# Kernel optimization log

Measured on AMD Instinct MI355X. Metric: run time of the kernel, lower is better.

## Reference

```python
import jax, jax.numpy as jnp
import numpy as np


def _conv(x, w, b=None, stride=1, pad=0):
    y = jax.lax.conv_general_dilated(x, w, (stride, stride), [(pad, pad), (pad, pad)],
                                     dimension_numbers=('NCHW', 'OIHW', 'NCHW'))
    if b is not None:
        y = y + b[None, :, None, None]
    return y


def _slice3d(grid, guide):
    # Trilinear grid_sample, align_corners=False, zero padding.
    # grid: (N, C=12, D=8, GH, GW); guide: (N,1,H,W) in [-1,1]
    N, C, D, GH, GW = grid.shape
    H, W = guide.shape[2], guide.shape[3]
    xs = 2.0 * jnp.arange(W, dtype=grid.dtype) / max(W - 1, 1) - 1.0
    ys = 2.0 * jnp.arange(H, dtype=grid.dtype) / max(H - 1, 1) - 1.0
    gx = ((xs + 1.0) * GW - 1.0) * 0.5               # (W,)
    gy = ((ys + 1.0) * GH - 1.0) * 0.5               # (H,)
    gz = ((guide[:, 0] + 1.0) * D - 1.0) * 0.5       # (N,H,W)
    x0f = jnp.floor(gx); y0f = jnp.floor(gy); z0f = jnp.floor(gz)
    fx = gx - x0f; fy = gy - y0f; fz = gz - z0f
    x0 = x0f.astype(jnp.int32); y0 = y0f.astype(jnp.int32); z0 = z0f.astype(jnp.int32)
    gf = grid.reshape(N, C, D * GH * GW)

    def corner(zi, yi, xi, wz, wy, wx):
        mask = ((zi >= 0) & (zi < D)) & ((yi >= 0) & (yi < GH))[None, :, None] & ((xi >= 0) & (xi < GW))[None, None, :]
        zc = jnp.clip(zi, 0, D - 1); yc = jnp.clip(yi, 0, GH - 1); xc = jnp.clip(xi, 0, GW - 1)
        flat = zc * (GH * GW) + yc[None, :, None] * GW + xc[None, None, :]   # (N,H,W)
        v = jnp.take_along_axis(gf, flat.reshape(N, 1, H * W), axis=2).reshape(N, C, H, W)
        w = (wz * wy[None, :, None] * wx[None, None, :]) * mask.astype(grid.dtype)  # (N,H,W)
        return v * w[:, None]

    out = jnp.zeros((N, C, H, W), grid.dtype)
    for dz in (0, 1):
        for dy in (0, 1):
            for dx in (0, 1):
                out = out + corner(z0 + dz, y0 + dy, x0 + dx,
                                   fz if dz else 1.0 - fz,
                                   fy if dy else 1.0 - fy,
                                   fx if dx else 1.0 - fx)
    return out


def setup_inputs() -> dict:
    key = jax.random.key(0)
    ks = jax.random.split(key, 40)
    def w(i, shape):
        return jax.random.normal(ks[i], shape, jnp.float32) * 0.05
    return {
        'low_res': jax.random.uniform(ks[0], (4, 3, 256, 256), jnp.float32),
        'full_res': jax.random.uniform(ks[1], (4, 1, 1024, 1024), jnp.float32),
        'w0': w(2, (8, 3, 3, 3)), 'b0': w(3, (8,)),
        'w1': w(4, (16, 8, 3, 3)), 'b1': w(5, (16,)),
        'w2': w(6, (32, 16, 3, 3)), 'b2': w(7, (32,)),
        'w3': w(8, (64, 32, 3, 3)), 'b3': w(9, (64,)),
        'wl0': w(10, (64, 64, 3, 3)), 'bl0': w(11, (64,)),
        'wl1': w(12, (64, 64, 3, 3)),
        'wg1': w(13, (128, 64, 3, 3)), 'bg1': w(14, (128,)),
        'wg2': w(15, (256, 128, 3, 3)), 'bg2': w(16, (256,)),
        'wf1': w(17, (256, 448, 1, 1)), 'bf1': w(18, (256,)),
        'wf2': w(19, (128, 256, 1, 1)), 'bf2': w(20, (128,)),
        'wf3': w(21, (64, 128, 1, 1)), 'bf3': w(22, (64,)),
        'wlin': w(23, (96, 64, 1, 1)), 'blin': w(24, (96,)),
        'wgd1': w(25, (16, 1, 3, 3)), 'bgd1': w(26, (16,)),
        'wgd2': w(27, (1, 16, 1, 1)), 'bgd2': w(28, (1,)),
        'wau1': w(29, (16, 1, 1, 1)), 'bau1': w(30, (16,)),
        'wau2': w(31, (1, 16, 1, 1)), 'bau2': w(32, (1,)),
        'wav1': w(33, (16, 1, 1, 1)), 'bav1': w(34, (16,)),
        'wav2': w(35, (1, 16, 1, 1)), 'bav2': w(36, (1,)),
    }


def reference(low_res, full_res, w0, b0, w1, b1, w2, b2, w3, b3, wl0, bl0, wl1,
              wg1, bg1, wg2, bg2, wf1, bf1, wf2, bf2, wf3, bf3, wlin, blin,
              wgd1, bgd1, wgd2, bgd2, wau1, bau1, wau2, bau2, wav1, bav1, wav2, bav2):
    relu = jax.nn.relu
    N = low_res.shape[0]
    H, W = full_res.shape[2], full_res.shape[3]
    fake = jax.image.resize(low_res, (N, 3, H, W), 'bilinear')
    # splat stack: 4 stride-2 convs
    x = relu(_conv(low_res, w0, b0, 2, 1))
    x = relu(_conv(x, w1, b1, 2, 1))
    x = relu(_conv(x, w2, b2, 2, 1))
    splat = relu(_conv(x, w3, b3, 2, 1))                 # (N,64,16,16)
    local = _conv(relu(_conv(splat, wl0, bl0, 1, 1)), wl1, None, 1, 1)
    # global branch
    a0 = splat.mean(axis=(2, 3), keepdims=True)
    x1 = relu(_conv(splat, wg1, bg1, 2, 1))
    a1 = x1.mean(axis=(2, 3), keepdims=True)
    x2 = relu(_conv(x1, wg2, bg2, 2, 1))
    a2 = x2.mean(axis=(2, 3), keepdims=True)
    a = jnp.concatenate([a0, a1, a2], axis=1)            # (N,448,1,1)
    a = relu(_conv(a, wf1, bf1))
    a = relu(_conv(a, wf2, bf2))
    glob = relu(_conv(a, wf3, bf3))                      # (N,64,1,1)
    fused = relu(glob + local)
    fused = _conv(fused, wlin, blin)                     # (N,96,16,16)
    grid = fused.reshape(N, 12, 8, fused.shape[2], fused.shape[3])
    guidemap = jnp.tanh(_conv(relu(_conv(full_res, wgd1, bgd1, 1, 1)), wgd2, bgd2))
    coeff = _slice3d(grid, guidemap)                     # (N,12,H,W)
    Y = full_res * coeff[:, 3:4] + coeff[:, 0:3].sum(axis=1, keepdims=True)
    U0 = full_res * coeff[:, 7:8] + coeff[:, 4:7].sum(axis=1, keepdims=True)
    V0 = full_res * coeff[:, 11:12] + coeff[:, 8:11].sum(axis=1, keepdims=True)
    U = jnp.tanh(_conv(relu(_conv(U0, wau1, bau1)), wau2, bau2)) + fake[:, 1:2]
    V = jnp.tanh(_conv(relu(_conv(V0, wav1, bav1)), wav2, bav2)) + fake[:, 2:3]
    return jnp.concatenate([Y, U, V], axis=1)
```

## Files before the change

### kernel.cpp

```cpp
#include <hip/hip_runtime.h>
#include <math.h>


__device__ __forceinline__ float tanh_fast(float x) {
    float e = __expf(2.0f * x);
    return 1.0f - 2.0f / (e + 1.0f);
}

template<int CIN, int COUT, int HIN, int WIN, int HOUT, int WOUT>
__global__ __launch_bounds__(256) void conv_s2_small(
    const float* __restrict__ in, const float* __restrict__ w,
    const float* __restrict__ b, float* __restrict__ out)
{
    int idx = blockIdx.x * 256 + threadIdx.x;
    int wo = idx % WOUT; int t = idx / WOUT;
    int ho = t % HOUT; t /= HOUT;
    int co = t % COUT; int n = t / COUT;
    float acc = b[co];
    int hi0 = ho * 2 - 1, wi0 = wo * 2 - 1;
    const float* wp = w + (size_t)co * CIN * 9;
    #pragma unroll
    for (int ci = 0; ci < CIN; ++ci) {
        const float* ip = in + ((size_t)(n * CIN + ci)) * HIN * WIN;
        const float* wc = wp + ci * 9;
        #pragma unroll
        for (int kh = 0; kh < 3; ++kh) {
            int hi = hi0 + kh;
            if ((unsigned)hi >= (unsigned)HIN) continue;
            const float* row = ip + hi * WIN;
            #pragma unroll
            for (int kw = 0; kw < 3; ++kw) {
                int wi = wi0 + kw;
                if ((unsigned)wi >= (unsigned)WIN) continue;
                acc = fmaf(wc[kh * 3 + kw], row[wi], acc);
            }
        }
    }
    out[idx] = fmaxf(acc, 0.0f);
}

template<int CIN, int PARTS, int STRIDE, bool RELU, bool HASB,
         int COUT, int HIN, int WIN, int HOUT, int WOUT>
__device__ __forceinline__ void conv_p_dev(
    const float* __restrict__ in, const float* __restrict__ w,
    const float* __restrict__ b, float* __restrict__ out,
    int tb, float* red)
{
    constexpr int CPT = CIN / PARTS;
    constexpr int OPB = 256 / PARTS;
    int part = threadIdx.x / OPB;
    int oidx = threadIdx.x % OPB;
    int o = tb * OPB + oidx;
    int wo = o % WOUT; int t = o / WOUT;
    int ho = t % HOUT; t /= HOUT;
    int co = t % COUT; int n = t / COUT;
    int hi0 = ho * STRIDE - 1, wi0 = wo * STRIDE - 1;
    const float* wp = w + ((size_t)co * CIN + part * CPT) * 9;
    const float* ip = in + ((size_t)n * CIN + part * CPT) * HIN * WIN;
    float acc = 0.0f;
    #pragma unroll
    for (int ci = 0; ci < CPT; ++ci) {
        const float* ic = ip + (size_t)ci * HIN * WIN;
        const float* wc = wp + ci * 9;
        #pragma unroll
        for (int kh = 0; kh < 3; ++kh) {
            int hi = hi0 + kh;
            if ((unsigned)hi >= (unsigned)HIN) continue;
            const float* row = ic + hi * WIN;
            #pragma unroll
            for (int kw = 0; kw < 3; ++kw) {
                int wi = wi0 + kw;
                if ((unsigned)wi >= (unsigned)WIN) continue;
                acc = fmaf(wc[kh * 3 + kw], row[wi], acc);
            }
        }
    }
    red[threadIdx.x] = acc;
    __syncthreads();
    if (part == 0) {
        float s = acc;
        #pragma unroll
        for (int p = 1; p < PARTS; ++p) s += red[p * OPB + oidx];
        if (HASB) s += b[co];
        if (RELU) s = fmaxf(s, 0.0f);
        out[o] = s;
    }
}

__global__ __launch_bounds__(256) void conv2_k(
    const float* __restrict__ in, const float* __restrict__ w,
    const float* __restrict__ b, float* __restrict__ out)
{
    __shared__ float red[256];
    conv_p_dev<16, 4, 2, true, true, 32, 64, 64, 32, 32>(in, w, b, out, blockIdx.x, red);
}

__global__ __launch_bounds__(256) void conv3_k(
    const float* __restrict__ in, const float* __restrict__ w,
    const float* __restrict__ b, float* __restrict__ out)
{
    __shared__ float red[256];
    conv_p_dev<32, 8, 2, true, true, 64, 32, 32, 16, 16>(in, w, b, out, blockIdx.x, red);
}

__global__ __launch_bounds__(256) void k5_l0_g1_means(
    const float* __restrict__ splat,
    const float* __restrict__ wl0, const float* __restrict__ bl0, float* __restrict__ l0o,
    const float* __restrict__ wg1, const float* __restrict__ bg1, float* __restrict__ x1,
    float* __restrict__ avec)
{
    __shared__ float red[256];
    int bid = blockIdx.x;
    if (bid < 4096) {
        conv_p_dev<64, 16, 1, true, true, 64, 16, 16, 16, 16>(splat, wl0, bl0, l0o, bid, red);
    } else if (bid < 6144) {
        conv_p_dev<64, 16, 2, true, true, 128, 16, 16, 8, 8>(splat, wg1, bg1, x1, bid - 4096, red);
    } else {
        int wid = (bid - 6144) * 4 + (threadIdx.x >> 6);
        int lane = threadIdx.x & 63;
        int n = wid >> 6, c = wid & 63;
        const float* p = splat + ((size_t)(n * 64 + c)) * 256;
        float s = p[lane] + p[lane + 64] + p[lane + 128] + p[lane + 192];
        #pragma unroll
        for (int off = 32; off; off >>= 1) s += __shfl_down(s, off, 64);
        if (lane == 0) avec[n * 448 + c] = s * (1.0f / 256.0f);
    }
}

__global__ __launch_bounds__(256) void k6_l1_g2_means(
    const float* __restrict__ l0o, const float* __restrict__ wl1, float* __restrict__ localb,
    const float* __restrict__ x1, const float* __restrict__ wg2,
    const float* __restrict__ bg2, float* __restrict__ x2,
    float* __restrict__ avec)
{
    __shared__ float red[256];
    int bid = blockIdx.x;
    if (bid < 4096) {
        conv_p_dev<64, 16, 1, false, false, 64, 16, 16, 16, 16>(l0o, wl1, nullptr, localb, bid, red);
    } else if (bid < 5120) {
        conv_p_dev<128, 16, 2, true, true, 256, 8, 8, 4, 4>(x1, wg2, bg2, x2, bid - 4096, red);
    } else {
        int wid = (bid - 5120) * 4 + (threadIdx.x >> 6);
        int lane = threadIdx.x & 63;
        int n = wid >> 7, c = wid & 127;
        const float* p = x1 + ((size_t)(n * 128 + c)) * 64;
        float s = p[lane];
        #pragma unroll
        for (int off = 32; off; off >>= 1) s += __shfl_down(s, off, 64);
        if (lane == 0) avec[n * 448 + 64 + c] = s * (1.0f / 64.0f);
    }
}

__global__ __launch_bounds__(256) void kfc_fuse(
    const float* __restrict__ avec, const float* __restrict__ x2,
    const float* __restrict__ wf1, const float* __restrict__ bf1,
    const float* __restrict__ wf2, const float* __restrict__ bf2,
    const float* __restrict__ wf3, const float* __restrict__ bf3,
    const float* __restrict__ local,
    const float* __restrict__ wlin, const float* __restrict__ blin,
    float* __restrict__ grid)
{
    __shared__ float a[448];
    __shared__ float h1[256];
    __shared__ float h2[128];
    __shared__ float gl[64];
    int n = blockIdx.x / 96; int k = blockIdx.x % 96; int t = threadIdx.x;
    if (t < 192) a[t] = avec[n * 448 + t];
    {
        const float* p = x2 + ((size_t)(n * 256 + t)) * 16;
        float s = 0.0f;
        #pragma unroll
        for (int i = 0; i < 16; ++i) s += p[i];
        a[192 + t] = s * (1.0f / 16.0f);
    }
    __syncthreads();
    {
        float a0 = 0, a1 = 0, a2 = 0, a3 = 0;
        const float* wp = wf1 + (size_t)t * 448;
        for (int i = 0; i < 448; i += 4) {
            a0 = fmaf(wp[i], a[i], a0); a1 = fmaf(wp[i + 1], a[i + 1], a1);
            a2 = fmaf(wp[i + 2], a[i + 2], a2); a3 = fmaf(wp[i + 3], a[i + 3], a3);
        }
        h1[t] = fmaxf(a0 + a1 + a2 + a3 + bf1[t], 0.0f);
    }
    __syncthreads();
    if (t < 128) {
        float a0 = 0, a1 = 0, a2 = 0, a3 = 0;
        const float* wp = wf2 + (size_t)t * 256;
        for (int i = 0; i < 256; i += 4) {
            a0 = fmaf(wp[i], h1[i], a0); a1 = fmaf(wp[i + 1], h1[i + 1], a1);
            a2 = fmaf(wp[i + 2], h1[i + 2], a2); a3 = fmaf(wp[i + 3], h1[i + 3], a3);
        }
        h2[t] = fmaxf(a0 + a1 + a2 + a3 + bf2[t], 0.0f);
    }
    __syncthreads();
    if (t < 64) {
        float a0 = 0, a1 = 0, a2 = 0, a3 = 0;
        const float* wp = wf3 + (size_t)t * 128;
        for (int i = 0; i < 128; i += 4) {
            a0 = fmaf(wp[i], h2[i], a0); a1 = fmaf(wp[i + 1], h2[i + 1], a1);
            a2 = fmaf(wp[i + 2], h2[i + 2], a2); a3 = fmaf(wp[i + 3], h2[i + 3], a3);
        }
        gl[t] = fmaxf(a0 + a1 + a2 + a3 + bf3[t], 0.0f);
    }
    __syncthreads();
    float acc = blin[k];
    const float* wp = wlin + k * 64;
    const float* lo = local + (size_t)n * 64 * 256 + t;
    #pragma unroll 8
    for (int c = 0; c < 64; ++c)
        acc = fmaf(wp[c], fmaxf(gl[c] + lo[c * 256], 0.0f), acc);
    int ch = k >> 3; int z = k & 7;
    grid[(((size_t)(n * 8 + z)) * 256 + t) * 12 + ch] = acc;
}

__global__ __launch_bounds__(256) void hdr_out_v2(
    const float* __restrict__ full, const float* __restrict__ low,
    const float* __restrict__ grid,
    const float* __restrict__ wgd1, const float* __restrict__ bgd1,
    const float* __restrict__ wgd2, const float* __restrict__ bgd2,
    const float* __restrict__ wau1, const float* __restrict__ bau1,
    const float* __restrict__ wau2, const float* __restrict__ bau2,
    const float* __restrict__ wav1, const float* __restrict__ bav1,
    const float* __restrict__ wav2, const float* __restrict__ bav2,
    float* __restrict__ out)
{
    int tid = blockIdx.x * 256 + threadIdx.x;
    int x0 = (tid & 255) << 2;
    int y = (tid >> 8) & 1023;
    int n = tid >> 18;
    const float* fp = full + ((size_t)n << 20);

    float v[3][6];
    #pragma unroll
    for (int r = 0; r < 3; ++r) {
        int yy = y + r - 1;
        bool okr = (unsigned)yy < 1024u;
        const float* row = fp + (size_t)yy * 1024;
        if (okr) {
            float4 m = *(const float4*)(row + x0);
            v[r][1] = m.x; v[r][2] = m.y; v[r][3] = m.z; v[r][4] = m.w;
            v[r][0] = (x0 > 0) ? row[x0 - 1] : 0.0f;
            v[r][5] = (x0 < 1020) ? row[x0 + 4] : 0.0f;
        } else {
            #pragma unroll
            for (int j = 0; j < 6; ++j) v[r][j] = 0.0f;
        }
    }

    float gacc[4];
    float bb = bgd2[0];
    #pragma unroll
    for (int px = 0; px < 4; ++px) gacc[px] = bb;
    #pragma unroll
    for (int k = 0; k < 16; ++k) {
        const float* wk = wgd1 + k * 9;
        float q0 = wk[0], q1 = wk[1], q2 = wk[2];
        float q3 = wk[3], q4 = wk[4], q5 = wk[5];
        float q6 = wk[6], q7 = wk[7], q8 = wk[8];
        float bk = bgd1[k], wo = wgd2[k];
        #pragma unroll
        for (int px = 0; px < 4; ++px) {
            float h = bk;
            h = fmaf(q0, v[0][px], h); h = fmaf(q1, v[0][px + 1], h); h = fmaf(q2, v[0][px + 2], h);
            h = fmaf(q3, v[1][px], h); h = fmaf(q4, v[1][px + 1], h); h = fmaf(q5, v[1][px + 2], h);
            h = fmaf(q6, v[2][px], h); h = fmaf(q7, v[2][px + 1], h); h = fmaf(q8, v[2][px + 2], h);
            gacc[px] = fmaf(wo, fmaxf(h, 0.0f), gacc[px]);
        }
    }

    const float* gbase = grid + (size_t)n * 24576;
    float Yo[4], Uo[4], Vo[4];

    #pragma unroll
    for (int px = 0; px < 4; ++px) {
        int x = x0 + px;
        float g = tanh_fast(gacc[px]);

        float gxc = (x * (32.0f / 1023.0f) - 1.0f) * 0.5f;
        float gyc = (y * (32.0f / 1023.0f) - 1.0f) * 0.5f;
        float gzc = 4.0f * g + 3.5f;
        float x0f = floorf(gxc), y0f = floorf(gyc), z0f = floorf(gzc);
        float fx = gxc - x0f, fy = gyc - y0f, fz = gzc - z0f;
        int ix = (int)x0f, iy = (int)y0f, iz = (int)z0f;

        float wx0 = (ix >= 0 && ix < 16) ? (1.0f - fx) : 0.0f;
        float wx1 = (ix + 1 < 16) ? fx : 0.0f;
        float wy0 = (iy >= 0 && iy < 16) ? (1.0f - fy) : 0.0f;
        float wy1 = (iy + 1 < 16) ? fy : 0.0f;
        float wz0 = (iz >= 0 && iz < 8) ? (1.0f - fz) : 0.0f;
        float wz1 = (iz + 1 >= 0 && iz + 1 < 8) ? fz : 0.0f;
        int xi0 = min(max(ix, 0), 15), xi1 = min(ix + 1, 15);
        int yi0 = min(max(iy, 0), 15), yi1 = min(iy + 1, 15);
        int zi0 = min(max(iz, 0), 7),  zi1 = min(max(iz + 1, 0), 7);

        float w00 = wy0 * wx0, w01 = wy0 * wx1, w10 = wy1 * wx0, w11 = wy1 * wx1;
        int o00 = yi0 * 16 + xi0, o01 = yi0 * 16 + xi1;
        int o10 = yi1 * 16 + xi0, o11 = yi1 * 16 + xi1;
        int z0b = zi0 * 256, z1b = zi1 * 256;

        float acc[12];
        #pragma unroll
        for (int i = 0; i < 12; ++i) acc[i] = 0.0f;

        #define CORNER(OFF, WK) { \
            const float4* q = (const float4*)(gbase + (size_t)(OFF) * 12); \
            float wk_ = (WK); \
            float4 A = q[0], B = q[1], C = q[2]; \
            acc[0] = fmaf(wk_, A.x, acc[0]); acc[1] = fmaf(wk_, A.y, acc[1]); \
            acc[2] = fmaf(wk_, A.z, acc[2]); acc[3] = fmaf(wk_, A.w, acc[3]); \
            acc[4] = fmaf(wk_, B.x, acc[4]); acc[5] = fmaf(wk_, B.y, acc[5]); \
            acc[6] = fmaf(wk_, B.z, acc[6]); acc[7] = fmaf(wk_, B.w, acc[7]); \
            acc[8] = fmaf(wk_, C.x, acc[8]); acc[9] = fmaf(wk_, C.y, acc[9]); \
            acc[10] = fmaf(wk_, C.z, acc[10]); acc[11] = fmaf(wk_, C.w, acc[11]); }

        CORNER(z0b + o00, wz0 * w00)
        CORNER(z0b + o01, wz0 * w01)
        CORNER(z0b + o10, wz0 * w10)
        CORNER(z0b + o11, wz0 * w11)
        CORNER(z1b + o00, wz1 * w00)
        CORNER(z1b + o01, wz1 * w01)
        CORNER(z1b + o10, wz1 * w10)
        CORNER(z1b + o11, wz1 * w11)
        #undef CORNER

        float p = v[1][px + 1];
        float Yv = fmaf(p, acc[3],  acc[0] + acc[1] + acc[2]);
        float U0 = fmaf(p, acc[7],  acc[4] + acc[5] + acc[6]);
        float V0 = fmaf(p, acc[11], acc[8] + acc[9] + acc[10]);

        float uacc = bau2[0];
        #pragma unroll
        for (int k = 0; k < 16; ++k)
            uacc = fmaf(wau2[k], fmaxf(fmaf(wau1[k], U0, bau1[k]), 0.0f), uacc);
        float vacc = bav2[0];
        #pragma unroll
        for (int k = 0; k < 16; ++k)
            vacc = fmaf(wav2[k], fmaxf(fmaf(wav1[k], V0, bav1[k]), 0.0f), vacc);

        float sx = (x + 0.5f) * 0.25f - 0.5f;
        float sy = (y + 0.5f) * 0.25f - 0.5f;
        float sxf = floorf(sx), syf = floorf(sy);
        float fxl = sx - sxf, fyl = sy - syf;
        int jx0 = max((int)sxf, 0), jx1 = min((int)sxf + 1, 255);
        int jy0 = max((int)syf, 0), jy1 = min((int)syf + 1, 255);
        const float* lr1 = low + ((size_t)(n * 3 + 1)) * 65536;
        const float* lr2 = low + ((size_t)(n * 3 + 2)) * 65536;
        float f1 = (1.0f - fyl) * ((1.0f - fxl) * lr1[jy0 * 256 + jx0] + fxl * lr1[jy0 * 256 + jx1])
                 + fyl * ((1.0f - fxl) * lr1[jy1 * 256 + jx0] + fxl * lr1[jy1 * 256 + jx1]);
        float f2 = (1.0f - fyl) * ((1.0f - fxl) * lr2[jy0 * 256 + jx0] + fxl * lr2[jy0 * 256 + jx1])
                 + fyl * ((1.0f - fxl) * lr2[jy1 * 256 + jx0] + fxl * lr2[jy1 * 256 + jx1]);

        Yo[px] = Yv;
        Uo[px] = tanh_fast(uacc) + f1;
        Vo[px] = tanh_fast(vacc) + f2;
    }

    size_t base = ((size_t)n * 3) * 1048576 + (size_t)y * 1024 + x0;
    *(float4*)(out + base)            = make_float4(Yo[0], Yo[1], Yo[2], Yo[3]);
    *(float4*)(out + base + 1048576)  = make_float4(Uo[0], Uo[1], Uo[2], Uo[3]);
    *(float4*)(out + base + 2097152)  = make_float4(Vo[0], Vo[1], Vo[2], Vo[3]);
}

extern "C" void kernel_launch(void* const* d_in, const int* in_sizes, int n_in,
                              void* d_out, int out_size, void* d_ws, size_t ws_size,
                              hipStream_t stream)
{
    const float* low  = (const float*)d_in[0];
    const float* full = (const float*)d_in[1];
    const float* w0 = (const float*)d_in[2];  const float* b0 = (const float*)d_in[3];
    const float* w1 = (const float*)d_in[4];  const float* b1 = (const float*)d_in[5];
    const float* w2 = (const float*)d_in[6];  const float* b2 = (const float*)d_in[7];
    const float* w3 = (const float*)d_in[8];  const float* b3 = (const float*)d_in[9];
    const float* wl0 = (const float*)d_in[10]; const float* bl0 = (const float*)d_in[11];
    const float* wl1 = (const float*)d_in[12];
    const float* wg1 = (const float*)d_in[13]; const float* bg1 = (const float*)d_in[14];
    const float* wg2 = (const float*)d_in[15]; const float* bg2 = (const float*)d_in[16];
    const float* wf1 = (const float*)d_in[17]; const float* bf1 = (const float*)d_in[18];
    const float* wf2 = (const float*)d_in[19]; const float* bf2 = (const float*)d_in[20];
    const float* wf3 = (const float*)d_in[21]; const float* bf3 = (const float*)d_in[22];
    const float* wlin = (const float*)d_in[23]; const float* blin = (const float*)d_in[24];
    const float* wgd1 = (const float*)d_in[25]; const float* bgd1 = (const float*)d_in[26];
    const float* wgd2 = (const float*)d_in[27]; const float* bgd2 = (const float*)d_in[28];
    const float* wau1 = (const float*)d_in[29]; const float* bau1 = (const float*)d_in[30];
    const float* wau2 = (const float*)d_in[31]; const float* bau2 = (const float*)d_in[32];
    const float* wav1 = (const float*)d_in[33]; const float* bav1 = (const float*)d_in[34];
    const float* wav2 = (const float*)d_in[35]; const float* bav2 = (const float*)d_in[36];
    float* out = (float*)d_out;

    float* ws = (float*)d_ws;
    float* t0b    = ws;
    float* t1b    = t0b + 524288;
    float* t2b    = t1b + 262144;
    float* splat  = t2b + 131072;
    float* l0o    = splat + 65536;
    float* localb = l0o + 65536;
    float* x1b    = localb + 65536;
    float* x2b    = x1b + 32768;
    float* avec   = x2b + 16384;
    float* gridb  = avec + 1792;

    conv_s2_small<3, 8, 256, 256, 128, 128><<<2048, 256, 0, stream>>>(low, w0, b0, t0b);
    conv_s2_small<8, 16, 128, 128, 64, 64><<<1024, 256, 0, stream>>>(t0b, w1, b1, t1b);
    conv2_k<<<2048, 256, 0, stream>>>(t1b, w2, b2, t2b);
    conv3_k<<<2048, 256, 0, stream>>>(t2b, w3, b3, splat);
    k5_l0_g1_means<<<6208, 256, 0, stream>>>(splat, wl0, bl0, l0o, wg1, bg1, x1b, avec);
    k6_l1_g2_means<<<5248, 256, 0, stream>>>(l0o, wl1, localb, x1b, wg2, bg2, x2b, avec);
    kfc_fuse<<<384, 256, 0, stream>>>(avec, x2b, wf1, bf1, wf2, bf2, wf3, bf3,
                                      localb, wlin, blin, gridb);
    hdr_out_v2<<<4096, 256, 0, stream>>>(full, low, gridb,
        wgd1, bgd1, wgd2, bgd2, wau1, bau1, wau2, bau2, wav1, bav1, wav2, bav2, out);
}
```

Baseline: 358.1 us.

## Store bilateral grid z-innermost and process one pixel per thread in output kernel

The grid written by the fuse kernel is re-laid out so that, for each spatial cell, all eight depth slices and twelve channels sit next to each other. This keeps the trilinear corner gathers in a small contiguous region per cell. The output kernel now handles one pixel per thread instead of four, launching four times as many blocks. This trades the float4 vectorized loads and stores and the reuse of weights and neighbouring pixels across four outputs for more parallelism and lower register pressure, which may improve occupancy.

```diff
diff --git a/kernel.cpp b/kernel.cpp
--- a/kernel.cpp
+++ b/kernel.cpp
@@ -211,10 +211,10 @@
     for (int c = 0; c < 64; ++c)
         acc = fmaf(wp[c], fmaxf(gl[c] + lo[c * 256], 0.0f), acc);
     int ch = k >> 3; int z = k & 7;
-    grid[(((size_t)(n * 8 + z)) * 256 + t) * 12 + ch] = acc;
-}
-
-__global__ __launch_bounds__(256) void hdr_out_v2(
+    grid[(size_t)n * 24576 + (size_t)t * 96 + z * 12 + ch] = acc;
+}
+
+__global__ __launch_bounds__(256) void hdr_out_v3(
     const float* __restrict__ full, const float* __restrict__ low,
     const float* __restrict__ grid,
     const float* __restrict__ wgd1, const float* __restrict__ bgd1,
@@ -226,140 +226,120 @@
     float* __restrict__ out)
 {
     int tid = blockIdx.x * 256 + threadIdx.x;
-    int x0 = (tid & 255) << 2;
-    int y = (tid >> 8) & 1023;
-    int n = tid >> 18;
+    int x = tid & 1023;
+    int y = (tid >> 10) & 1023;
+    int n = tid >> 20;
     const float* fp = full + ((size_t)n << 20);
 
-    float v[3][6];
+    float v[3][3];
     #pragma unroll
     for (int r = 0; r < 3; ++r) {
         int yy = y + r - 1;
         bool okr = (unsigned)yy < 1024u;
         const float* row = fp + (size_t)yy * 1024;
-        if (okr) {
-            float4 m = *(const float4*)(row + x0);
-            v[r][1] = m.x; v[r][2] = m.y; v[r][3] = m.z; v[r][4] = m.w;
-            v[r][0] = (x0 > 0) ? row[x0 - 1] : 0.0f;
-            v[r][5] = (x0 < 1020) ? row[x0 + 4] : 0.0f;
-        } else {
-            #pragma unroll
-            for (int j = 0; j < 6; ++j) v[r][j] = 0.0f;
-        }
-    }
-
-    float gacc[4];
-    float bb = bgd2[0];
-    #pragma unroll
-    for (int px = 0; px < 4; ++px) gacc[px] = bb;
+        v[r][0] = (okr && x > 0)    ? row[x - 1] : 0.0f;
+        v[r][1] = okr               ? row[x]     : 0.0f;
+        v[r][2] = (okr && x < 1023) ? row[x + 1] : 0.0f;
+    }
+
+    float gacc = bgd2[0];
     #pragma unroll
     for (int k = 0; k < 16; ++k) {
         const float* wk = wgd1 + k * 9;
-        float q0 = wk[0], q1 = wk[1], q2 = wk[2];
-        float q3 = wk[3], q4 = wk[4], q5 = wk[5];
-        float q6 = wk[6], q7 = wk[7], q8 = wk[8];
-        float bk = bgd1[k], wo = wgd2[k];
-        #pragma unroll
-        for (int px = 0; px < 4; ++px) {
-            float h = bk;
-            h = fmaf(q0, v[0][px], h); h = fmaf(q1, v[0][px + 1], h); h = fmaf(q2, v[0][px + 2], h);
-            h = fmaf(q3, v[1][px], h); h = fmaf(q4, v[1][px + 1], h); h = fmaf(q5, v[1][px + 2], h);
-            h = fmaf(q6, v[2][px], h); h = fmaf(q7, v[2][px + 1], h); h = fmaf(q8, v[2][px + 2], h);
-            gacc[px] = fmaf(wo, fmaxf(h, 0.0f), gacc[px]);
-        }
-    }
-
-    const float* gbase = grid + (size_t)n * 24576;
-    float Yo[4], Uo[4], Vo[4];
-
-    #pragma unroll
-    for (int px = 0; px < 4; ++px) {
-        int x = x0 + px;
-        float g = tanh_fast(gacc[px]);
-
-        float gxc = (x * (32.0f / 1023.0f) - 1.0f) * 0.5f;
-        float gyc = (y * (32.0f / 1023.0f) - 1.0f) * 0.5f;
-        float gzc = 4.0f * g + 3.5f;
-        float x0f = floorf(gxc), y0f = floorf(gyc), z0f = floorf(gzc);
-        float fx = gxc - x0f, fy = gyc - y0f, fz = gzc - z0f;
-        int ix = (int)x0f, iy = (int)y0f, iz = (int)z0f;
-
-        float wx0 = (ix >= 0 && ix < 16) ? (1.0f - fx) : 0.0f;
-        float wx1 = (ix + 1 < 16) ? fx : 0.0f;
-        float wy0 = (iy >= 0 && iy < 16) ? (1.0f - fy) : 0.0f;
-        float wy1 = (iy + 1 < 16) ? fy : 0.0f;
-        float wz0 = (iz >= 0 && iz < 8) ? (1.0f - fz) : 0.0f;
-        float wz1 = (iz + 1 >= 0 && iz + 1 < 8) ? fz : 0.0f;
-        int xi0 = min(max(ix, 0), 15), xi1 = min(ix + 1, 15);
-        int yi0 = min(max(iy, 0), 15), yi1 = min(iy + 1, 15);
-        int zi0 = min(max(iz, 0), 7),  zi1 = min(max(iz + 1, 0), 7);
-
-        float w00 = wy0 * wx0, w01 = wy0 * wx1, w10 = wy1 * wx0, w11 = wy1 * wx1;
-        int o00 = yi0 * 16 + xi0, o01 = yi0 * 16 + xi1;
-        int o10 = yi1 * 16 + xi0, o11 = yi1 * 16 + xi1;
-        int z0b = zi0 * 256, z1b = zi1 * 256;
-
-        float acc[12];
-        #pragma unroll
-        for (int i = 0; i < 12; ++i) acc[i] = 0.0f;
-
-        #define CORNER(OFF, WK) { \
-            const float4* q = (const float4*)(gbase + (size_t)(OFF) * 12); \
-            float wk_ = (WK); \
-            float4 A = q[0], B = q[1], C = q[2]; \
-            acc[0] = fmaf(wk_, A.x, acc[0]); acc[1] = fmaf(wk_, A.y, acc[1]); \
-            acc[2] = fmaf(wk_, A.z, acc[2]); acc[3] = fmaf(wk_, A.w, acc[3]); \
-            acc[4] = fmaf(wk_, B.x, acc[4]); acc[5] = fmaf(wk_, B.y, acc[5]); \
-            acc[6] = fmaf(wk_, B.z, acc[6]); acc[7] = fmaf(wk_, B.w, acc[7]); \
-            acc[8] = fmaf(wk_, C.x, acc[8]); acc[9] = fmaf(wk_, C.y, acc[9]); \
-            acc[10] = fmaf(wk_, C.z, acc[10]); acc[11] = fmaf(wk_, C.w, acc[11]); }
-
-        CORNER(z0b + o00, wz0 * w00)
-        CORNER(z0b + o01, wz0 * w01)
-        CORNER(z0b + o10, wz0 * w10)
-        CORNER(z0b + o11, wz0 * w11)
-        CORNER(z1b + o00, wz1 * w00)
-        CORNER(z1b + o01, wz1 * w01)
-        CORNER(z1b + o10, wz1 * w10)
-        CORNER(z1b + o11, wz1 * w11)
-        #undef CORNER
-
-        float p = v[1][px + 1];
-        float Yv = fmaf(p, acc[3],  acc[0] + acc[1] + acc[2]);
-        float U0 = fmaf(p, acc[7],  acc[4] + acc[5] + acc[6]);
-        float V0 = fmaf(p, acc[11], acc[8] + acc[9] + acc[10]);
-
-        float uacc = bau2[0];
-        #pragma unroll
-        for (int k = 0; k < 16; ++k)
-            uacc = fmaf(wau2[k], fmaxf(fmaf(wau1[k], U0, bau1[k]), 0.0f), uacc);
-        float vacc = bav2[0];
-        #pragma unroll
-        for (int k = 0; k < 16; ++k)
-            vacc = fmaf(wav2[k], fmaxf(fmaf(wav1[k], V0, bav1[k]), 0.0f), vacc);
-
-        float sx = (x + 0.5f) * 0.25f - 0.5f;
-        float sy = (y + 0.5f) * 0.25f - 0.5f;
-        float sxf = floorf(sx), syf = floorf(sy);
-        float fxl = sx - sxf, fyl = sy - syf;
-        int jx0 = max((int)sxf, 0), jx1 = min((int)sxf + 1, 255);
-        int jy0 = max((int)syf, 0), jy1 = min((int)syf + 1, 255);
-        const float* lr1 = low + ((size_t)(n * 3 + 1)) * 65536;
-        const float* lr2 = low + ((size_t)(n * 3 + 2)) * 65536;
-        float f1 = (1.0f - fyl) * ((1.0f - fxl) * lr1[jy0 * 256 + jx0] + fxl * lr1[jy0 * 256 + jx1])
-                 + fyl * ((1.0f - fxl) * lr1[jy1 * 256 + jx0] + fxl * lr1[jy1 * 256 + jx1]);
-        float f2 = (1.0f - fyl) * ((1.0f - fxl) * lr2[jy0 * 256 + jx0] + fxl * lr2[jy0 * 256 + jx1])
-                 + fyl * ((1.0f - fxl) * lr2[jy1 * 256 + jx0] + fxl * lr2[jy1 * 256 + jx1]);
-
-        Yo[px] = Yv;
-        Uo[px] = tanh_fast(uacc) + f1;
-        Vo[px] = tanh_fast(vacc) + f2;
-    }
-
-    size_t base = ((size_t)n * 3) * 1048576 + (size_t)y * 1024 + x0;
-    *(float4*)(out + base)            = make_float4(Yo[0], Yo[1], Yo[2], Yo[3]);
-    *(float4*)(out + base + 1048576)  = make_float4(Uo[0], Uo[1], Uo[2], Uo[3]);
-    *(float4*)(out + base + 2097152)  = make_float4(Vo[0], Vo[1], Vo[2], Vo[3]);
+        float h = bgd1[k];
+        h = fmaf(wk[0], v[0][0], h); h = fmaf(wk[1], v[0][1], h); h = fmaf(wk[2], v[0][2], h);
+        h = fmaf(wk[3], v[1][0], h); h = fmaf(wk[4], v[1][1], h); h = fmaf(wk[5], v[1][2], h);
+        h = fmaf(wk[6], v[2][0], h); h = fmaf(wk[7], v[2][1], h); h = fmaf(wk[8], v[2][2], h);
+        gacc = fmaf(wgd2[k], fmaxf(h, 0.0f), gacc);
+    }
+    float g = tanh_fast(gacc);
+
+    float gxc = (x * (32.0f / 1023.0f) - 1.0f) * 0.5f;
+    float gyc = (y * (32.0f / 1023.0f) - 1.0f) * 0.5f;
+    float gzc = 4.0f * g + 3.5f;
+    float x0f = floorf(gxc), y0f = floorf(gyc), z0f = floorf(gzc);
+    float fx = gxc - x0f, fy = gyc - y0f, fz = gzc - z0f;
+    int ix = (int)x0f, iy = (int)y0f, iz = (int)z0f;
+
+    float wx0 = (ix >= 0 && ix < 16) ? (1.0f - fx) : 0.0f;
+    float wx1 = (ix + 1 < 16) ? fx : 0.0f;
+    float wy0 = (iy >= 0 && iy < 16) ? (1.0f - fy) : 0.0f;
+    float wy1 = (iy + 1 < 16) ? fy : 0.0f;
+    float wz0 = (iz >= 0 && iz < 8) ? (1.0f - fz) : 0.0f;
+    float wz1 = (iz + 1 >= 0 && iz + 1 < 8) ? fz : 0.0f;
+    int xi0 = min(max(ix, 0), 15), xi1 = min(ix + 1, 15);
+    int yi0 = min(max(iy, 0), 15), yi1 = min(iy + 1, 15);
+    int zi0 = min(max(iz, 0), 7),  zi1 = min(max(iz + 1, 0), 7);
+
+    float w00 = wy0 * wx0, w01 = wy0 * wx1, w10 = wy1 * wx0, w11 = wy1 * wx1;
+
+    const float* gb = grid + (size_t)n * 24576;
+    const float* c00 = gb + (yi0 * 16 + xi0) * 96;
+    const float* c01 = gb + (yi0 * 16 + xi1) * 96;
+    const float* c10 = gb + (yi1 * 16 + xi0) * 96;
+    const float* c11 = gb + (yi1 * 16 + xi1) * 96;
+    int zo0 = zi0 * 12;
+    int zo1 = zi1 * 12;
+
+    float acc[12];
+    #pragma unroll
+    for (int i = 0; i < 12; ++i) acc[i] = 0.0f;
+
+    #define CORNER(PTR, WK) { \
+        const float4* q = (const float4*)(PTR); \
+        float wk_ = (WK); \
+        float4 A = q[0], B = q[1], C = q[2]; \
+        acc[0] = fmaf(wk_, A.x, acc[0]); acc[1] = fmaf(wk_, A.y, acc[1]); \
+        acc[2] = fmaf(wk_, A.z, acc[2]); acc[3] = fmaf(wk_, A.w, acc[3]); \
+        acc[4] = fmaf(wk_, B.x, acc[4]); acc[5] = fmaf(wk_, B.y, acc[5]); \
+        acc[6] = fmaf(wk_, B.z, acc[6]); acc[7] = fmaf(wk_, B.w, acc[7]); \
+        acc[8] = fmaf(wk_, C.x, acc[8]); acc[9] = fmaf(wk_, C.y, acc[9]); \
+        acc[10] = fmaf(wk_, C.z, acc[10]); acc[11] = fmaf(wk_, C.w, acc[11]); }
+
+    CORNER(c00 + zo0, wz0 * w00)
+    CORNER(c01 + zo0, wz0 * w01)
+    CORNER(c10 + zo0, wz0 * w10)
+    CORNER(c11 + zo0, wz0 * w11)
+    CORNER(c00 + zo1, wz1 * w00)
+    CORNER(c01 + zo1, wz1 * w01)
+    CORNER(c10 + zo1, wz1 * w10)
+    CORNER(c11 + zo1, wz1 * w11)
+    #undef CORNER
+
+    float p = v[1][1];
+    float Yv = fmaf(p, acc[3],  acc[0] + acc[1] + acc[2]);
+    float U0 = fmaf(p, acc[7],  acc[4] + acc[5] + acc[6]);
+    float V0 = fmaf(p, acc[11], acc[8] + acc[9] + acc[10]);
+
+    float uacc = bau2[0];
+    #pragma unroll
+    for (int k = 0; k < 16; ++k)
+        uacc = fmaf(wau2[k], fmaxf(fmaf(wau1[k], U0, bau1[k]), 0.0f), uacc);
+    float vacc = bav2[0];
+    #pragma unroll
+    for (int k = 0; k < 16; ++k)
+        vacc = fmaf(wav2[k], fmaxf(fmaf(wav1[k], V0, bav1[k]), 0.0f), vacc);
+
+    float sx = (x + 0.5f) * 0.25f - 0.5f;
+    float sy = (y + 0.5f) * 0.25f - 0.5f;
+    float sxf = floorf(sx), syf = floorf(sy);
+    float fxl = sx - sxf, fyl = sy - syf;
+    int jx0 = max((int)sxf, 0), jx1 = min((int)sxf + 1, 255);
+    int jy0 = max((int)syf, 0), jy1 = min((int)syf + 1, 255);
+    const float* lr1 = low + ((size_t)(n * 3 + 1)) * 65536;
+    const float* lr2 = low + ((size_t)(n * 3 + 2)) * 65536;
+    float f1 = (1.0f - fyl) * ((1.0f - fxl) * lr1[jy0 * 256 + jx0] + fxl * lr1[jy0 * 256 + jx1])
+             + fyl * ((1.0f - fxl) * lr1[jy1 * 256 + jx0] + fxl * lr1[jy1 * 256 + jx1]);
+    float f2 = (1.0f - fyl) * ((1.0f - fxl) * lr2[jy0 * 256 + jx0] + fxl * lr2[jy0 * 256 + jx1])
+             + fyl * ((1.0f - fxl) * lr2[jy1 * 256 + jx0] + fxl * lr2[jy1 * 256 + jx1]);
+
+    float Uv = tanh_fast(uacc) + f1;
+    float Vv = tanh_fast(vacc) + f2;
+
+    size_t base = ((size_t)n * 3) * 1048576 + (size_t)y * 1024 + x;
+    out[base]            = Yv;
+    out[base + 1048576]  = Uv;
+    out[base + 2097152]  = Vv;
 }
 
 extern "C" void kernel_launch(void* const* d_in, const int* in_sizes, int n_in,
@@ -408,6 +388,6 @@
     k6_l1_g2_means<<<5248, 256, 0, stream>>>(l0o, wl1, localb, x1b, wg2, bg2, x2b, avec);
     kfc_fuse<<<384, 256, 0, stream>>>(avec, x2b, wf1, bf1, wf2, bf2, wf3, bf3,
                                       localb, wlin, blin, gridb);
-    hdr_out_v2<<<4096, 256, 0, stream>>>(full, low, gridb,
+    hdr_out_v3<<<16384, 256, 0, stream>>>(full, low, gridb,
         wgd1, bgd1, wgd2, bgd2, wau1, bau1, wau2, bau2, wav1, bav1, wav2, bav2, out);
 }
```

Measured after the change: 352.2 us. No clear change (-1.7%).
